# Performance work log

Measured on AMD Instinct MI355X. Metric: run time of the kernel, lower is better.

Reference implementation:

```python
import jax, jax.numpy as jnp
import numpy as np

N_CLUSTERS = 1024


def setup_inputs() -> dict:
    key = jax.random.key(0)
    k1, k2 = jax.random.split(key)
    batch = jax.random.normal(k1, (262144, 64), dtype=jnp.float32)
    centroids = jax.random.normal(k2, (N_CLUSTERS, 64), dtype=jnp.float32)
    return {"batch": batch, "centroids": centroids}


def reference(batch, centroids):
    x_sq = jnp.sum(batch * batch, axis=1, keepdims=True)          # [N, 1]
    c_sq = jnp.sum(centroids * centroids, axis=1)                 # [K]
    cross = batch @ centroids.T                                   # [N, K]
    distances = x_sq - 2.0 * cross + c_sq[None, :]
    assignments = jnp.argmin(distances, axis=1)                   # [N] int
    # Counts and sums via scatter-add (avoids materializing one-hot [N, K])
    batch_cluster_counts = jnp.zeros((N_CLUSTERS,), dtype=jnp.int32).at[assignments].add(1)
    batch_cluster_sums = jax.ops.segment_sum(batch, assignments, num_segments=N_CLUSTERS)  # [K, D]
    return (assignments, batch_cluster_counts, batch_cluster_sums)
```

## Files before the change

### kernel.cpp

```cpp
#include <hip/hip_runtime.h>
#include <float.h>

#define N_PTS 262144
#define K_CL  1024
#define D     64
#define PTS_PER_WAVE   64
#define WAVES_PER_BLK  16
#define PTS_PER_BLK    (PTS_PER_WAVE * WAVES_PER_BLK)
#define NTILE 8
#define MARGIN_S 0.5f
#define CAND_CAP 6

typedef _Float16 f16;
typedef _Float16 half8 __attribute__((ext_vector_type(8)));
typedef float    f32x4 __attribute__((ext_vector_type(4)));

__global__ __launch_bounds__(256) void prep_kernel(const float* __restrict__ cent,
                                                   float* __restrict__ csq,
                                                   float* __restrict__ csqhn,
                                                   f16* __restrict__ cent16) {
    int k = blockIdx.x * 256 + threadIdx.x;
    if (k >= K_CL) return;
    const float* row = &cent[(size_t)k * D];
    float s = 0.f;
    #pragma unroll
    for (int d = 0; d < D; ++d) s = fmaf(row[d], row[d], s);
    csq[k]   = s;
    csqhn[k] = -0.5f * s;
    int sw = k & 7;
    #pragma unroll
    for (int ch = 0; ch < 8; ++ch) {
        half8 h;
        #pragma unroll
        for (int e = 0; e < 8; ++e) h[e] = (f16)row[ch * 8 + e];
        *reinterpret_cast<half8*>(&cent16[(size_t)k * D + (size_t)((ch ^ sw) * 8)]) = h;
    }
}

__device__ __forceinline__ float exact_dist(const float* __restrict__ xr,
                                            const float* __restrict__ cr,
                                            float xsq, float cs) {
    float dot = 0.f;
    #pragma unroll
    for (int d = 0; d < D; ++d) dot = fmaf(xr[d], cr[d], dot);
    return (xsq - 2.0f * dot) + cs;
}

__device__ __forceinline__ half8 point_frag(const float* __restrict__ batch,
                                            int prow, int chunk) {
    const float* src = &batch[(size_t)prow * D + chunk * 8];
    float4 u0 = *reinterpret_cast<const float4*>(src);
    float4 u1 = *reinterpret_cast<const float4*>(src + 4);
    half8 h;
    h[0] = (f16)u0.x; h[1] = (f16)u0.y; h[2] = (f16)u0.z; h[3] = (f16)u0.w;
    h[4] = (f16)u1.x; h[5] = (f16)u1.y; h[6] = (f16)u1.z; h[7] = (f16)u1.w;
    return h;
}

__device__ __forceinline__ float vmax4(const f32x4& a) {
    return fmaxf(fmaxf(a.x, a.y), fmaxf(a.z, a.w));
}

__device__ __forceinline__ void collect(const f32x4& a, float thr, int cbase, int& cnt,
                                        int& s0, int& s1, int& s2, int& s3, int& s4, int& s5) {
    if (vmax4(a) >= thr) {
        #pragma unroll
        for (int r = 0; r < 4; ++r) {
            if (a[r] >= thr) {
                int c = cbase + r;
                if      (cnt == 0) s0 = c;
                else if (cnt == 1) s1 = c;
                else if (cnt == 2) s2 = c;
                else if (cnt == 3) s3 = c;
                else if (cnt == 4) s4 = c;
                else if (cnt == 5) s5 = c;
                cnt++;
            }
        }
    }
}

__device__ __forceinline__ void resolve(const float* __restrict__ batch,
                                        const float* __restrict__ cent,
                                        const float* __restrict__ csq,
                                        int prow, int hi, int cnt,
                                        int s0, int s1, int s2, int s3, int s4, int s5,
                                        float& bd, int& bi) {
    bd = FLT_MAX; bi = 0x7fffffff;
    if (cnt == 0) return;
    const float* xr = &batch[(size_t)prow * D];
    float xsq = 0.f;
    #pragma unroll
    for (int d = 0; d < D; ++d) xsq = fmaf(xr[d], xr[d], xsq);
    if (cnt <= CAND_CAP) {
        #pragma unroll
        for (int r = 0; r < CAND_CAP; ++r) {
            int c = (r == 0) ? s0 : (r == 1) ? s1 : (r == 2) ? s2
                  : (r == 3) ? s3 : (r == 4) ? s4 : s5;
            if (r < cnt) {
                float dd = exact_dist(xr, &cent[(size_t)c * D], xsq, csq[c]);
                if (dd < bd || (dd == bd && c < bi)) { bd = dd; bi = c; }
            }
        }
    } else {
        for (int t16 = 0; t16 < 64; ++t16) {
            #pragma unroll
            for (int r = 0; r < 4; ++r) {
                int c = t16 * 16 + hi * 4 + r;
                float dd = exact_dist(xr, &cent[(size_t)c * D], xsq, csq[c]);
                if (dd < bd || (dd == bd && c < bi)) { bd = dd; bi = c; }
            }
        }
    }
}

__global__ __launch_bounds__(1024, 4) void assign_kernel(
    const float* __restrict__ batch,
    const f16*   __restrict__ cent16,
    const float* __restrict__ csq,
    const float* __restrict__ csqhn,
    const float* __restrict__ cent,
    float* __restrict__ out_assign,
    float* __restrict__ ps_base,
    float* __restrict__ cs_base,
    int split_mask)
{
    __shared__ f16   C16[K_CL * D];
    __shared__ __align__(16) float CH[K_CL];

    const int tid   = threadIdx.x;
    const int wave  = tid >> 6;
    const int lane  = tid & 63;
    const int lo    = lane & 15;
    const int hi    = lane >> 4;
    const int wbase = (blockIdx.x * WAVES_PER_BLK + wave) * PTS_PER_WAVE;

    #pragma unroll
    for (int it = 0; it < 8; ++it) {
        int u = tid + 1024 * it;
        *reinterpret_cast<half8*>(&C16[u * 8]) =
            *reinterpret_cast<const half8*>(&cent16[(size_t)u * 8]);
    }
    CH[tid] = csqhn[tid];
    __syncthreads();

    const int pr0 = wbase + 0 * 16 + lo;
    const int pr1 = wbase + 1 * 16 + lo;
    const int pr2 = wbase + 2 * 16 + lo;
    const int pr3 = wbase + 3 * 16 + lo;

    const half8 p0a = point_frag(batch, pr0, hi), p0b = point_frag(batch, pr0, 4 + hi);
    const half8 p1a = point_frag(batch, pr1, hi), p1b = point_frag(batch, pr1, 4 + hi);
    const half8 p2a = point_frag(batch, pr2, hi), p2b = point_frag(batch, pr2, 4 + hi);
    const half8 p3a = point_frag(batch, pr3, hi), p3b = point_frag(batch, pr3, 4 + hi);

    float m0 = -FLT_MAX, m1 = -FLT_MAX, m2 = -FLT_MAX, m3 = -FLT_MAX;
    for (int t = 0; t < NTILE; ++t) {
        const int base = t * 128;
        #pragma unroll
        for (int m = 0; m < 8; ++m) {
            const int row = base + m * 16 + lo;
            const int sw  = row & 7;
            const half8 cf0 = *reinterpret_cast<const half8*>(&C16[row * D + ((hi     ^ sw) * 8)]);
            const half8 cf1 = *reinterpret_cast<const half8*>(&C16[row * D + (((4+hi) ^ sw) * 8)]);
            const f32x4 ch  = *reinterpret_cast<const f32x4*>(&CH[base + m * 16 + hi * 4]);
            f32x4 a0 = ch, a1 = ch, a2 = ch, a3 = ch;
            a0 = __builtin_amdgcn_mfma_f32_16x16x32_f16(cf0, p0a, a0, 0, 0, 0);
            a0 = __builtin_amdgcn_mfma_f32_16x16x32_f16(cf1, p0b, a0, 0, 0, 0);
            a1 = __builtin_amdgcn_mfma_f32_16x16x32_f16(cf0, p1a, a1, 0, 0, 0);
            a1 = __builtin_amdgcn_mfma_f32_16x16x32_f16(cf1, p1b, a1, 0, 0, 0);
            a2 = __builtin_amdgcn_mfma_f32_16x16x32_f16(cf0, p2a, a2, 0, 0, 0);
            a2 = __builtin_amdgcn_mfma_f32_16x16x32_f16(cf1, p2b, a2, 0, 0, 0);
            a3 = __builtin_amdgcn_mfma_f32_16x16x32_f16(cf0, p3a, a3, 0, 0, 0);
            a3 = __builtin_amdgcn_mfma_f32_16x16x32_f16(cf1, p3b, a3, 0, 0, 0);
            m0 = fmaxf(m0, vmax4(a0));
            m1 = fmaxf(m1, vmax4(a1));
            m2 = fmaxf(m2, vmax4(a2));
            m3 = fmaxf(m3, vmax4(a3));
        }
    }
    m0 = fmaxf(m0, __shfl_xor(m0, 16)); m0 = fmaxf(m0, __shfl_xor(m0, 32));
    m1 = fmaxf(m1, __shfl_xor(m1, 16)); m1 = fmaxf(m1, __shfl_xor(m1, 32));
    m2 = fmaxf(m2, __shfl_xor(m2, 16)); m2 = fmaxf(m2, __shfl_xor(m2, 32));
    m3 = fmaxf(m3, __shfl_xor(m3, 16)); m3 = fmaxf(m3, __shfl_xor(m3, 32));
    const float t0 = m0 - MARGIN_S, t1 = m1 - MARGIN_S,
                t2 = m2 - MARGIN_S, t3 = m3 - MARGIN_S;

    int n0 = 0, n1 = 0, n2 = 0, n3 = 0;
    int a0c0=0,a0c1=0,a0c2=0,a0c3=0,a0c4=0,a0c5=0;
    int a1c0=0,a1c1=0,a1c2=0,a1c3=0,a1c4=0,a1c5=0;
    int a2c0=0,a2c1=0,a2c2=0,a2c3=0,a2c4=0,a2c5=0;
    int a3c0=0,a3c1=0,a3c2=0,a3c3=0,a3c4=0,a3c5=0;

    for (int t = 0; t < NTILE; ++t) {
        const int base = t * 128;
        #pragma unroll
        for (int m = 0; m < 8; ++m) {
            const int row = base + m * 16 + lo;
            const int sw  = row & 7;
            const half8 cf0 = *reinterpret_cast<const half8*>(&C16[row * D + ((hi     ^ sw) * 8)]);
            const half8 cf1 = *reinterpret_cast<const half8*>(&C16[row * D + (((4+hi) ^ sw) * 8)]);
            const f32x4 ch  = *reinterpret_cast<const f32x4*>(&CH[base + m * 16 + hi * 4]);
            f32x4 a0 = ch, a1 = ch, a2 = ch, a3 = ch;
            a0 = __builtin_amdgcn_mfma_f32_16x16x32_f16(cf0, p0a, a0, 0, 0, 0);
            a0 = __builtin_amdgcn_mfma_f32_16x16x32_f16(cf1, p0b, a0, 0, 0, 0);
            a1 = __builtin_amdgcn_mfma_f32_16x16x32_f16(cf0, p1a, a1, 0, 0, 0);
            a1 = __builtin_amdgcn_mfma_f32_16x16x32_f16(cf1, p1b, a1, 0, 0, 0);
            a2 = __builtin_amdgcn_mfma_f32_16x16x32_f16(cf0, p2a, a2, 0, 0, 0);
            a2 = __builtin_amdgcn_mfma_f32_16x16x32_f16(cf1, p2b, a2, 0, 0, 0);
            a3 = __builtin_amdgcn_mfma_f32_16x16x32_f16(cf0, p3a, a3, 0, 0, 0);
            a3 = __builtin_amdgcn_mfma_f32_16x16x32_f16(cf1, p3b, a3, 0, 0, 0);
            const int cbase = base + m * 16 + hi * 4;
            collect(a0, t0, cbase, n0, a0c0, a0c1, a0c2, a0c3, a0c4, a0c5);
            collect(a1, t1, cbase, n1, a1c0, a1c1, a1c2, a1c3, a1c4, a1c5);
            collect(a2, t2, cbase, n2, a2c0, a2c1, a2c2, a2c3, a2c4, a2c5);
            collect(a3, t3, cbase, n3, a3c0, a3c1, a3c2, a3c3, a3c4, a3c5);
        }
    }

    float bd0, bd1, bd2, bd3;
    int   bi0, bi1, bi2, bi3;
    resolve(batch, cent, csq, pr0, hi, n0, a0c0, a0c1, a0c2, a0c3, a0c4, a0c5, bd0, bi0);
    resolve(batch, cent, csq, pr1, hi, n1, a1c0, a1c1, a1c2, a1c3, a1c4, a1c5, bd1, bi1);
    resolve(batch, cent, csq, pr2, hi, n2, a2c0, a2c1, a2c2, a2c3, a2c4, a2c5, bd2, bi2);
    resolve(batch, cent, csq, pr3, hi, n3, a3c0, a3c1, a3c2, a3c3, a3c4, a3c5, bd3, bi3);

    #pragma unroll
    for (int off = 16; off <= 32; off <<= 1) {
        float od; int oi;
        od = __shfl_xor(bd0, off); oi = __shfl_xor(bi0, off);
        if (od < bd0 || (od == bd0 && oi < bi0)) { bd0 = od; bi0 = oi; }
        od = __shfl_xor(bd1, off); oi = __shfl_xor(bi1, off);
        if (od < bd1 || (od == bd1 && oi < bi1)) { bd1 = od; bi1 = oi; }
        od = __shfl_xor(bd2, off); oi = __shfl_xor(bi2, off);
        if (od < bd2 || (od == bd2 && oi < bi2)) { bd2 = od; bi2 = oi; }
        od = __shfl_xor(bd3, off); oi = __shfl_xor(bi3, off);
        if (od < bd3 || (od == bd3 && oi < bi3)) { bd3 = od; bi3 = oi; }
    }

    if (hi == 0) {
        out_assign[pr0] = (float)bi0;
        out_assign[pr1] = (float)bi1;
        out_assign[pr2] = (float)bi2;
        out_assign[pr3] = (float)bi3;
    }

    const int split = (blockIdx.x * WAVES_PER_BLK + wave) & split_mask;
    float* ps = ps_base + (size_t)split * K_CL * D;
    float* cs = cs_base + (size_t)split * K_CL;
    #pragma unroll 4
    for (int s = 0; s < 4; ++s) {
        int bis = (s == 0) ? bi0 : (s == 1) ? bi1 : (s == 2) ? bi2 : bi3;
        for (int p = 0; p < 16; ++p) {
            int a = __shfl(bis, p);
            int pt = wbase + s * 16 + p;
            float v = batch[(size_t)pt * D + lane];
            atomicAdd(&ps[(size_t)a * D + lane], v);
            if (lane == 0) atomicAdd(&cs[a], 1.0f);
        }
    }
}

__global__ __launch_bounds__(256) void reduce_kernel(
    const float* __restrict__ partial,
    const float* __restrict__ cnt_partial,
    float* __restrict__ out_counts,
    float* __restrict__ out_sums,
    int nsplit)
{
    int idx = blockIdx.x * 256 + threadIdx.x;
    if (idx < K_CL * D) {
        float s = 0.f;
        for (int e = 0; e < nsplit; ++e) s += partial[(size_t)e * K_CL * D + idx];
        out_sums[idx] = s;
    } else if (idx < K_CL * D + K_CL) {
        int c = idx - K_CL * D;
        float s = 0.f;
        for (int e = 0; e < nsplit; ++e) s += cnt_partial[e * K_CL + c];
        out_counts[c] = s;
    }
}

extern "C" void kernel_launch(void* const* d_in, const int* in_sizes, int n_in,
                              void* d_out, int out_size, void* d_ws, size_t ws_size,
                              hipStream_t stream) {
    const float* batch = (const float*)d_in[0];
    const float* cent  = (const float*)d_in[1];
    float* out        = (float*)d_out;
    float* out_assign = out;
    float* out_counts = out + N_PTS;
    float* out_sums   = out + N_PTS + K_CL;

    float* csq    = (float*)d_ws;
    float* csqhn  = csq + K_CL;
    f16*   cent16 = (f16*)((char*)d_ws + 8192);
    float* partial = (float*)((char*)d_ws + 8192 + 131072);

    int nsplit = 0;
    for (int ns = 32; ns >= 2; ns >>= 1) {
        size_t need = 8192 + 131072 +
                      (size_t)ns * K_CL * D * 4 + (size_t)ns * K_CL * 4;
        if (ws_size >= need) { nsplit = ns; break; }
    }

    prep_kernel<<<K_CL / 256, 256, 0, stream>>>(cent, csq, csqhn, cent16);

    if (nsplit > 0) {
        float* cnt_partial = partial + (size_t)nsplit * K_CL * D;
        hipMemsetAsync(partial, 0,
                       (size_t)(nsplit * K_CL * D + nsplit * K_CL) * sizeof(float), stream);
        assign_kernel<<<N_PTS / PTS_PER_BLK, 1024, 0, stream>>>(
            batch, cent16, csq, csqhn, cent, out_assign,
            partial, cnt_partial, nsplit - 1);
        reduce_kernel<<<(K_CL * D + K_CL + 255) / 256, 256, 0, stream>>>(
            partial, cnt_partial, out_counts, out_sums, nsplit);
    } else {
        hipMemsetAsync(out_counts, 0, (size_t)(K_CL + K_CL * D) * sizeof(float), stream);
        assign_kernel<<<N_PTS / PTS_PER_BLK, 1024, 0, stream>>>(
            batch, cent16, csq, csqhn, cent, out_assign,
            out_sums, out_counts, 0);
    }
}
```

Measured before the change: 188.9 us.

## Replace fused atomic segment-sum with counting-sort gather reduction

Moves the per-cluster sum and count out of the assign kernel. A histogram, a scan, an index placement and a per-cluster gather-sum now replace the float atomics into split partial buffers and their reduction. This removes heavy contended atomicAdd traffic and the memset and reduce of large partial arrays. In exchange it adds several launches and a second pass that rereads the batch with random row gathers, and float summation order now depends on placement.

```diff
diff --git a/kernel.cpp b/kernel.cpp
--- a/kernel.cpp
+++ b/kernel.cpp
@@ -120,10 +120,7 @@
     const float* __restrict__ csq,
     const float* __restrict__ csqhn,
     const float* __restrict__ cent,
-    float* __restrict__ out_assign,
-    float* __restrict__ ps_base,
-    float* __restrict__ cs_base,
-    int split_mask)
+    float* __restrict__ out_assign)
 {
     __shared__ f16   C16[K_CL * D];
     __shared__ __align__(16) float CH[K_CL];
@@ -244,40 +241,88 @@
         out_assign[pr2] = (float)bi2;
         out_assign[pr3] = (float)bi3;
     }
-
-    const int split = (blockIdx.x * WAVES_PER_BLK + wave) & split_mask;
-    float* ps = ps_base + (size_t)split * K_CL * D;
-    float* cs = cs_base + (size_t)split * K_CL;
+}
+
+__global__ __launch_bounds__(256) void hist_kernel(const float* __restrict__ assignF,
+                                                   int* __restrict__ hist) {
+    int t = blockIdx.x * 256 + threadIdx.x;
+    float4 av = *reinterpret_cast<const float4*>(&assignF[(size_t)t * 4]);
+    atomicAdd(&hist[(int)av.x], 1);
+    atomicAdd(&hist[(int)av.y], 1);
+    atomicAdd(&hist[(int)av.z], 1);
+    atomicAdd(&hist[(int)av.w], 1);
+}
+
+__global__ __launch_bounds__(1024) void scan_kernel(const int* __restrict__ hist,
+                                                    int* __restrict__ offsets,
+                                                    float* __restrict__ out_counts) {
+    __shared__ int tmp[1024];
+    const int t = threadIdx.x;
+    const int v = hist[t];
+    tmp[t] = v;
+    out_counts[t] = (float)v;
+    for (int off = 1; off < 1024; off <<= 1) {
+        __syncthreads();
+        int add = (t >= off) ? tmp[t - off] : 0;
+        __syncthreads();
+        tmp[t] += add;
+    }
+    __syncthreads();
+    offsets[t] = tmp[t] - v;
+}
+
+__global__ __launch_bounds__(256) void place_kernel(const float* __restrict__ assignF,
+                                                    const int* __restrict__ offsets,
+                                                    int* __restrict__ cursor,
+                                                    int* __restrict__ idx_sorted) {
+    int t = blockIdx.x * 256 + threadIdx.x;
+    float4 av = *reinterpret_cast<const float4*>(&assignF[(size_t)t * 4]);
+    #pragma unroll
+    for (int j = 0; j < 4; ++j) {
+        int a = (int)((j == 0) ? av.x : (j == 1) ? av.y : (j == 2) ? av.z : av.w);
+        int slot = atomicAdd(&cursor[a], 1);
+        idx_sorted[offsets[a] + slot] = t * 4 + j;
+    }
+}
+
+__global__ __launch_bounds__(256) void gather_sum_kernel(const float* __restrict__ batch,
+                                                         const int* __restrict__ hist,
+                                                         const int* __restrict__ offsets,
+                                                         const int* __restrict__ idx_sorted,
+                                                         float* __restrict__ out_sums) {
+    const int c    = blockIdx.x;
+    const int wave = threadIdx.x >> 6;
+    const int lane = threadIdx.x & 63;
+    const int n    = hist[c];
+    const int off  = offsets[c];
+    float acc = 0.f;
+    for (int i = wave; i < n; i += 4) {
+        int p = idx_sorted[off + i];
+        acc += batch[(size_t)p * D + lane];
+    }
+    __shared__ float part[4][64];
+    part[wave][lane] = acc;
+    __syncthreads();
+    if (wave == 0) {
+        out_sums[(size_t)c * D + lane] =
+            part[0][lane] + part[1][lane] + part[2][lane] + part[3][lane];
+    }
+}
+
+__global__ __launch_bounds__(256) void scatter_atomic_kernel(
+    const float* __restrict__ batch,
+    const float* __restrict__ assignF,
+    float* __restrict__ out_counts,
+    float* __restrict__ out_sums)
+{
+    const int gwave = (blockIdx.x * 256 + threadIdx.x) >> 6;
+    const int lane  = threadIdx.x & 63;
     #pragma unroll 4
-    for (int s = 0; s < 4; ++s) {
-        int bis = (s == 0) ? bi0 : (s == 1) ? bi1 : (s == 2) ? bi2 : bi3;
-        for (int p = 0; p < 16; ++p) {
-            int a = __shfl(bis, p);
-            int pt = wbase + s * 16 + p;
-            float v = batch[(size_t)pt * D + lane];
-            atomicAdd(&ps[(size_t)a * D + lane], v);
-            if (lane == 0) atomicAdd(&cs[a], 1.0f);
-        }
-    }
-}
-
-__global__ __launch_bounds__(256) void reduce_kernel(
-    const float* __restrict__ partial,
-    const float* __restrict__ cnt_partial,
-    float* __restrict__ out_counts,
-    float* __restrict__ out_sums,
-    int nsplit)
-{
-    int idx = blockIdx.x * 256 + threadIdx.x;
-    if (idx < K_CL * D) {
-        float s = 0.f;
-        for (int e = 0; e < nsplit; ++e) s += partial[(size_t)e * K_CL * D + idx];
-        out_sums[idx] = s;
-    } else if (idx < K_CL * D + K_CL) {
-        int c = idx - K_CL * D;
-        float s = 0.f;
-        for (int e = 0; e < nsplit; ++e) s += cnt_partial[e * K_CL + c];
-        out_counts[c] = s;
+    for (int it = 0; it < 16; ++it) {
+        int p = gwave * 16 + it;
+        int a = (int)assignF[p];
+        if (lane == 0) atomicAdd(&out_counts[a], 1.0f);
+        atomicAdd(&out_sums[(size_t)a * D + lane], batch[(size_t)p * D + lane]);
     }
 }
 
@@ -291,33 +336,32 @@
     float* out_counts = out + N_PTS;
     float* out_sums   = out + N_PTS + K_CL;
 
-    float* csq    = (float*)d_ws;
-    float* csqhn  = csq + K_CL;
-    f16*   cent16 = (f16*)((char*)d_ws + 8192);
-    float* partial = (float*)((char*)d_ws + 8192 + 131072);
-
-    int nsplit = 0;
-    for (int ns = 32; ns >= 2; ns >>= 1) {
-        size_t need = 8192 + 131072 +
-                      (size_t)ns * K_CL * D * 4 + (size_t)ns * K_CL * 4;
-        if (ws_size >= need) { nsplit = ns; break; }
-    }
+    char* ws = (char*)d_ws;
+    float* csq    = (float*)ws;
+    float* csqhn  = (float*)(ws + 4096);
+    f16*   cent16 = (f16*)(ws + 8192);
+    int*   hist       = (int*)(ws + 8192 + 131072);
+    int*   offsets    = hist + K_CL;
+    int*   cursor     = offsets + K_CL;
+    int*   idx_sorted = cursor + K_CL;
+
+    const size_t need = 8192 + 131072 + 3 * K_CL * 4 + (size_t)N_PTS * 4;
 
     prep_kernel<<<K_CL / 256, 256, 0, stream>>>(cent, csq, csqhn, cent16);
-
-    if (nsplit > 0) {
-        float* cnt_partial = partial + (size_t)nsplit * K_CL * D;
-        hipMemsetAsync(partial, 0,
-                       (size_t)(nsplit * K_CL * D + nsplit * K_CL) * sizeof(float), stream);
-        assign_kernel<<<N_PTS / PTS_PER_BLK, 1024, 0, stream>>>(
-            batch, cent16, csq, csqhn, cent, out_assign,
-            partial, cnt_partial, nsplit - 1);
-        reduce_kernel<<<(K_CL * D + K_CL + 255) / 256, 256, 0, stream>>>(
-            partial, cnt_partial, out_counts, out_sums, nsplit);
+    assign_kernel<<<N_PTS / PTS_PER_BLK, 1024, 0, stream>>>(
+        batch, cent16, csq, csqhn, cent, out_assign);
+
+    if (ws_size >= need) {
+        hipMemsetAsync(hist, 0, 2 * K_CL * sizeof(int), stream);
+        hipMemsetAsync(cursor, 0, K_CL * sizeof(int), stream);
+        hist_kernel<<<N_PTS / (4 * 256), 256, 0, stream>>>((const float*)out_assign, hist);
+        scan_kernel<<<1, 1024, 0, stream>>>(hist, offsets, out_counts);
+        place_kernel<<<N_PTS / (4 * 256), 256, 0, stream>>>(
+            (const float*)out_assign, offsets, cursor, idx_sorted);
+        gather_sum_kernel<<<K_CL, 256, 0, stream>>>(batch, hist, offsets, idx_sorted, out_sums);
     } else {
         hipMemsetAsync(out_counts, 0, (size_t)(K_CL + K_CL * D) * sizeof(float), stream);
-        assign_kernel<<<N_PTS / PTS_PER_BLK, 1024, 0, stream>>>(
-            batch, cent16, csq, csqhn, cent, out_assign,
-            out_sums, out_counts, 0);
-    }
-}
+        scatter_atomic_kernel<<<N_PTS / (16 * 4), 256, 0, stream>>>(
+            batch, out_assign, out_counts, out_sums);
+    }
+}
```

After: 717.9 us. 3.8x slower.
